# Kernel optimization log

Measured on AMD Instinct MI355X. Metric: run time of the kernel, lower is better.

The kernel has to match this reference:

```python
import jax, jax.numpy as jnp
import numpy as np

N, D, B, NMAX, H = 6144, 512, 16, 512, 8
HD = D // H
LARGE = 1e10
EPS = 1e-5


def setup_inputs() -> dict:
    key = jax.random.key(0)
    ks = jax.random.split(key, 20)
    s = 0.02
    inp = {
        'h': jax.random.normal(ks[0], (N, D), jnp.float32),
        'batch': jnp.sort(jax.random.randint(ks[1], (N,), 0, B)),
        # attention projections (stored as [in, out])
        'Wq': jax.random.normal(ks[2], (D, D), jnp.float32) * s,
        'bq': jnp.zeros((D,), jnp.float32),
        'Wk': jax.random.normal(ks[3], (D, D), jnp.float32) * s,
        'bk': jnp.zeros((D,), jnp.float32),
        'Wv': jax.random.normal(ks[4], (D, D), jnp.float32) * s,
        'bv': jnp.zeros((D,), jnp.float32),
        'Wo': jax.random.normal(ks[5], (D, D), jnp.float32) * s,
        'bo': jnp.zeros((D,), jnp.float32),
        # batchnorm 1 (after attention residual)
        'g1': jnp.ones((D,), jnp.float32),
        'be1': jnp.zeros((D,), jnp.float32),
        # FFN
        'W1': jax.random.normal(ks[6], (D, 2 * D), jnp.float32) * s,
        'b1': jnp.zeros((2 * D,), jnp.float32),
        'W2': jax.random.normal(ks[7], (2 * D, D), jnp.float32) * s,
        'b2': jnp.zeros((D,), jnp.float32),
        # batchnorm 2 (after FFN residual)
        'g2': jnp.ones((D,), jnp.float32),
        'be2': jnp.zeros((D,), jnp.float32),
    }
    return inp


def _batchnorm(x, g, b):
    # BatchNorm1d in training mode: batch statistics over the node dim
    m = jnp.mean(x, axis=0)
    v = jnp.var(x, axis=0)
    return (x - m) * jax.lax.rsqrt(v + EPS) * g + b


def reference(h, batch, Wq, bq, Wk, bk, Wv, bv, Wo, bo, g1, be1, W1, b1, W2, b2, g2, be2):
    # to_dense_batch: batch is sorted graph ids -> position within each graph
    starts = jnp.searchsorted(batch, jnp.arange(B))
    pos = jnp.arange(h.shape[0]) - starts[batch]
    hd = jnp.zeros((B, NMAX, D), h.dtype).at[batch, pos].set(h)
    mask = jnp.zeros((B, NMAX), bool).at[batch, pos].set(True)

    # attention (note reshape splits hidden as [head_dim, head], faithful to torch code)
    q = (hd @ Wq + bq).reshape(B, NMAX, HD, H)
    k = (hd @ Wk + bk).reshape(B, NMAX, HD, H)
    v = (hd @ Wv + bv).reshape(B, NMAX, HD, H)
    score = jnp.einsum('bnfh,bmfh->bnmh', k, q) / (HD ** 0.5)
    score = score - (~mask)[:, None, :, None].astype(score.dtype) * LARGE
    attn = jax.nn.softmax(score, axis=2)
    av = jnp.einsum('bnmh,bmfh->bnfh', attn, v).reshape(B, NMAX, D)
    out = av @ Wo + bo

    # back to flat node list (dense[mask]) + residual + BN
    h_attn = out[batch, pos]
    h_attn = h + h_attn
    h_attn = _batchnorm(h_attn, g1, be1)

    # FFN + residual + BN
    ff = jax.nn.relu(h_attn @ W1 + b1) @ W2 + b2
    return _batchnorm(h_attn + ff, g2, be2)
```

## Files before the change

kernel.cpp:

```cpp
#include <hip/hip_runtime.h>
#include <stdint.h>

#define N_NODES 6144
#define DIM 512
#define NGRAPH 16
#define NHEAD 8
#define EPSV 1e-5f

typedef unsigned short u16;
typedef short s16x4 __attribute__((ext_vector_type(4)));
typedef short s16x8 __attribute__((ext_vector_type(8)));
typedef __bf16 bf16x8 __attribute__((ext_vector_type(8)));
typedef float f32x4 __attribute__((ext_vector_type(4)));

__device__ __forceinline__ u16 f2bf(float f) {
  union { float f; unsigned u; } c{f};
  unsigned u = c.u;
  return (u16)((u + 0x7fffu + ((u >> 16) & 1u)) >> 16);
}
__device__ __forceinline__ float bf2f(u16 v) {
  union { unsigned u; float f; } c{(unsigned)v << 16};
  return c.f;
}

__device__ __forceinline__ f32x4 mfma16(s16x8 a, s16x8 b, f32x4 c) {
  return __builtin_amdgcn_mfma_f32_16x16x32_bf16(
      __builtin_bit_cast(bf16x8, a), __builtin_bit_cast(bf16x8, b), c, 0, 0, 0);
}

__device__ __forceinline__ void gload_lds16(const void* g, void* l) {
  __builtin_amdgcn_global_load_lds(
      (const __attribute__((address_space(1))) unsigned int*)g,
      (__attribute__((address_space(3))) unsigned int*)l, 16, 0, 0);
}

__device__ __forceinline__ s16x8 v_frag_tr(const u16* base, int u16idx) {
  s16x4 lo, hi;
  const __attribute__((address_space(3))) u16* p =
      (const __attribute__((address_space(3))) u16*)(base + u16idx);
  asm volatile("ds_read_b64_tr_b16 %0, %2\n\t"
               "ds_read_b64_tr_b16 %1, %2 offset:128\n\t"
               "s_waitcnt lgkmcnt(0)"
               : "=&v"(lo), "=&v"(hi)
               : "v"(p)
               : "memory");
  __builtin_amdgcn_sched_barrier(0);
  s16x8 r;
  r[0] = lo[0]; r[1] = lo[1]; r[2] = lo[2]; r[3] = lo[3];
  r[4] = hi[0]; r[5] = hi[1]; r[6] = hi[2]; r[7] = hi[3];
  return r;
}

__global__ void prep_kernel(const float* __restrict__ h, const int* __restrict__ batch,
                            const float* __restrict__ Wq, const float* __restrict__ Wk,
                            const float* __restrict__ Wv, const float* __restrict__ Wo,
                            const float* __restrict__ W1, const float* __restrict__ W2,
                            u16* __restrict__ bt_qkv, u16* __restrict__ bt_o,
                            u16* __restrict__ bt_1, u16* __restrict__ bt_2,
                            u16* __restrict__ A0, int* __restrict__ starts) {
  __shared__ float tile[32][33];
  const int bid = blockIdx.x, tid = threadIdx.x;
  if (bid == 0) {
    int g = tid;
    if (g > NGRAPH) return;
    if (g == NGRAPH) { starts[g] = N_NODES; return; }
    int lo = 0, hi = N_NODES;
    while (lo < hi) { int mid = (lo + hi) >> 1; if (batch[mid] < g) lo = mid + 1; else hi = mid; }
    starts[g] = lo;
    return;
  }
  if (bid >= 2049) {
    int i = (bid - 2049) * 256 + tid;
    float4 v = ((const float4*)h)[i];
    ushort4 o = make_ushort4(f2bf(v.x), f2bf(v.y), f2bf(v.z), f2bf(v.w));
    ((ushort4*)A0)[i] = o;
    return;
  }
  const int tx = tid & 31, ty = tid >> 5;
  if (bid <= 768) {
    const int w = (bid - 1) >> 8;
    const float* src = (w == 0) ? Wq : (w == 1) ? Wk : Wv;
    u16* dst = bt_qkv + (size_t)w * 512 * 512;
    const int t = (bid - 1) & 255;
    const int c0 = (t & 15) * 32, r0 = (t >> 4) * 32;
#pragma unroll
    for (int i = 0; i < 32; i += 8) tile[ty + i][tx] = src[(size_t)(r0 + ty + i) * 512 + c0 + tx];
    __syncthreads();
#pragma unroll
    for (int i = 0; i < 32; i += 8) {
      int c = c0 + ty + i;
      int v = ((c & 7) << 6) | (c >> 3);
      dst[(size_t)v * 512 + r0 + tx] = f2bf(tile[tx][ty + i]);
    }
  } else if (bid <= 1024) {
    const int t = bid - 769;
    const int c0 = (t & 15) * 32, j0 = (t >> 4) * 32;
#pragma unroll
    for (int i = 0; i < 32; i += 8) {
      int c = c0 + ty + i;
      int md = ((c & 63) << 3) | (c >> 6);
      tile[ty + i][tx] = Wo[(size_t)md * 512 + j0 + tx];
    }
    __syncthreads();
#pragma unroll
    for (int i = 0; i < 32; i += 8)
      bt_o[(size_t)(j0 + ty + i) * 512 + c0 + tx] = f2bf(tile[tx][ty + i]);
  } else if (bid <= 1536) {
    const int t = bid - 1025;
    const int c0 = (t & 31) * 32, r0 = (t >> 5) * 32;
#pragma unroll
    for (int i = 0; i < 32; i += 8) tile[ty + i][tx] = W1[(size_t)(r0 + ty + i) * 1024 + c0 + tx];
    __syncthreads();
#pragma unroll
    for (int i = 0; i < 32; i += 8) bt_1[(size_t)(c0 + ty + i) * 512 + r0 + tx] = f2bf(tile[tx][ty + i]);
  } else {
    const int t = bid - 1537;
    const int c0 = (t & 15) * 32, r0 = (t >> 4) * 32;
#pragma unroll
    for (int i = 0; i < 32; i += 8) tile[ty + i][tx] = W2[(size_t)(r0 + ty + i) * 512 + c0 + tx];
    __syncthreads();
#pragma unroll
    for (int i = 0; i < 32; i += 8) bt_2[(size_t)(c0 + ty + i) * 1024 + r0 + tx] = f2bf(tile[tx][ty + i]);
  }
}

template <int BM, int BN, int EPI>
__global__ __launch_bounds__(256, 2) void gemm_kernel(
    const u16* __restrict__ A, const u16* __restrict__ Bt,
    const float* __restrict__ bias0, const float* __restrict__ bias1,
    const float* __restrict__ bias2, const float* __restrict__ resf,
    const u16* __restrict__ resb, float2* __restrict__ part,
    u16* __restrict__ oq, u16* __restrict__ ok, u16* __restrict__ ov,
    float* __restrict__ of, u16* __restrict__ ob, int M, int N, int K) {
  constexpr int NW_M = (BM >= 128) ? 2 : 1;
  constexpr int NW_N = 4 / NW_M;
  constexpr int WM = BM / NW_M, WN = BN / NW_N;
  constexpr int FM = WM / 16, FN = WN / 16;
  __shared__ __align__(16) u16 As[BM * 64];
  __shared__ __align__(16) u16 Bs[BN * 64];
  const int tid = threadIdx.x;
  const int lane = tid & 63, wv = tid >> 6;
  const int wm = wv / NW_N, wn = wv % NW_N;
  const int row0 = blockIdx.y * BM, col0 = blockIdx.x * BN;

  f32x4 acc[FM][FN] = {};
  int a_off[FM], b_off[FN];
#pragma unroll
  for (int fm = 0; fm < FM; ++fm) {
    int r = wm * WM + fm * 16 + (lane & 15);
    a_off[fm] = r * 32 + (((lane >> 4) ^ ((r >> 1) & 3)) << 3);
  }
#pragma unroll
  for (int fn = 0; fn < FN; ++fn) {
    int r = wn * WN + fn * 16 + (lane & 15);
    b_off[fn] = r * 32 + (((lane >> 4) ^ ((r >> 1) & 3)) << 3);
  }

  for (int k0 = 0; k0 < K; k0 += 64) {
    __syncthreads();
#pragma unroll
    for (int is = 0; is < BM / 32; ++is) {
      int s = is * 256 + tid;
      int kh = s / (BM * 4);
      int sh = s - kh * (BM * 4);
      int r = sh >> 2;
      int cl = (sh & 3) ^ ((r >> 1) & 3);
      gload_lds16(A + (size_t)(row0 + r) * K + k0 + kh * 32 + cl * 8,
                  (void*)(As + (size_t)(is * 256 + (tid & ~63)) * 8));
    }
#pragma unroll
    for (int is = 0; is < BN / 32; ++is) {
      int s = is * 256 + tid;
      int kh = s / (BN * 4);
      int sh = s - kh * (BN * 4);
      int r = sh >> 2;
      int cl = (sh & 3) ^ ((r >> 1) & 3);
      gload_lds16(Bt + (size_t)(col0 + r) * K + k0 + kh * 32 + cl * 8,
                  (void*)(Bs + (size_t)(is * 256 + (tid & ~63)) * 8));
    }
    __syncthreads();
#pragma unroll
    for (int kh = 0; kh < 2; ++kh) {
      s16x8 af[FM], bfv[FN];
#pragma unroll
      for (int fm = 0; fm < FM; ++fm) af[fm] = *(const s16x8*)(As + kh * (BM * 32) + a_off[fm]);
#pragma unroll
      for (int fn = 0; fn < FN; ++fn) bfv[fn] = *(const s16x8*)(Bs + kh * (BN * 32) + b_off[fn]);
#pragma unroll
      for (int fm = 0; fm < FM; ++fm)
#pragma unroll
        for (int fn = 0; fn < FN; ++fn)
          acc[fm][fn] = mfma16(af[fm], bfv[fn], acc[fm][fn]);
    }
  }

  if constexpr (EPI == 0) {
    const int which = col0 >> 9;
    u16* dst = (which == 0) ? oq : (which == 1) ? ok : ov;
    const float* bias = (which == 0) ? bias0 : (which == 1) ? bias1 : bias2;
#pragma unroll
    for (int fn = 0; fn < FN; ++fn) {
      const int j = col0 + wn * WN + fn * 16 + (lane & 15);
      const int v = j & 511;
      const float bj = bias[((v & 63) << 3) | (v >> 6)];
#pragma unroll
      for (int fm = 0; fm < FM; ++fm) {
        const int ibase = row0 + wm * WM + fm * 16 + ((lane >> 4) << 2);
#pragma unroll
        for (int ii = 0; ii < 4; ++ii)
          dst[(size_t)(ibase + ii) * 512 + v] = f2bf(acc[fm][fn][ii] + bj);
      }
    }
  } else {
#pragma unroll
    for (int fn = 0; fn < FN; ++fn) {
      const int j = col0 + wn * WN + fn * 16 + (lane & 15);
      const float bj = bias0[j];
      float s = 0.f, q = 0.f;
#pragma unroll
      for (int fm = 0; fm < FM; ++fm) {
        const int ibase = row0 + wm * WM + fm * 16 + ((lane >> 4) << 2);
        if constexpr (EPI == 1) {
#pragma unroll
          for (int ii = 0; ii < 4; ++ii) {
            int i = ibase + ii;
            float val = acc[fm][fn][ii] + bj + resf[(size_t)i * N + j];
            ob[(size_t)i * N + j] = f2bf(val);
            s += val; q += val * val;
          }
        } else if constexpr (EPI == 2) {
#pragma unroll
          for (int ii = 0; ii < 4; ++ii) {
            int i = ibase + ii;
            float v = acc[fm][fn][ii] + bj;
            ob[(size_t)i * N + j] = f2bf(v > 0.f ? v : 0.f);
          }
        } else {
#pragma unroll
          for (int ii = 0; ii < 4; ++ii) {
            int i = ibase + ii;
            float val = acc[fm][fn][ii] + bj + bf2f(resb[(size_t)i * N + j]);
            of[(size_t)i * N + j] = val;
            s += val; q += val * val;
          }
        }
      }
      if constexpr (EPI == 1 || EPI == 3) {
        s += __shfl_xor(s, 16); s += __shfl_xor(s, 32);
        q += __shfl_xor(q, 16); q += __shfl_xor(q, 32);
        if ((lane >> 4) == 0) part[(size_t)blockIdx.y * 512 + j] = make_float2(s, q);
      }
    }
  }
}

__global__ __launch_bounds__(256, 2) void attn_kernel(
    const u16* __restrict__ qp, const u16* __restrict__ kp,
    const u16* __restrict__ vp, const int* __restrict__ starts,
    u16* __restrict__ av) {
  __shared__ __align__(16) u16 Qs[32 * 64];
  __shared__ __align__(16) u16 Vs[32 * 64];
  __shared__ __align__(16) u16 Ps[4][512];
  const int idx = blockIdx.x;
  const int rb = idx & 7, hh = (idx >> 3) & 7, b = idx >> 6;
  const int base = starts[b], nb = starts[b + 1] - base;
  const int r0 = rb * 64;
  if (r0 >= nb) return;
  const int tid = threadIdx.x, lane = tid & 63, wv = tid >> 6;
  const int g = lane >> 4;
  const int rloc = r0 + wv * 16 + (lane & 15);
  const u16* krow = kp + (size_t)(base + rloc) * 512 + hh * 64 + (g << 3);
  s16x8 ak0 = *(const s16x8*)(krow);
  s16x8 ak1 = *(const s16x8*)(krow + 32);
  f32x4 acc_av[4] = {};
  float rs[4] = {0.f, 0.f, 0.f, 0.f};
  u16* Pw = Ps[wv];
  const int vm = ((tid & 63) >> 3) * 4 + ((tid >> 1) & 3);
  const int vf = wv * 16 + (tid & 1) * 8;

  for (int m0 = 0; m0 < nb; m0 += 32) {
    __syncthreads();
    {
      int r = tid >> 3, cl = (tid & 7) ^ (r & 7);
      gload_lds16(qp + (size_t)(base + m0 + r) * 512 + hh * 64 + cl * 8,
                  (void*)(Qs + (size_t)(tid & ~63) * 8));
    }
    {
      gload_lds16(vp + (size_t)(base + m0 + vm) * 512 + hh * 64 + vf,
                  (void*)(Vs + (size_t)(tid & ~63) * 8));
    }
    __syncthreads();
#pragma unroll
    for (int ch = 0; ch < 2; ++ch) {
      f32x4 s = {};
#pragma unroll
      for (int kc = 0; kc < 2; ++kc) {
        const int mr = ch * 16 + (lane & 15);
        const int chunk = kc * 4 + g;
        s16x8 bq = *(const s16x8*)(Qs + mr * 64 + ((chunk ^ (mr & 7)) << 3));
        s = mfma16(kc == 0 ? ak0 : ak1, bq, s);
      }
      const int mg = m0 + ch * 16 + (lane & 15);
      const bool valid = mg < nb;
      const int c = ch * 16 + (lane & 15);
#pragma unroll
      for (int ii = 0; ii < 4; ++ii) {
        float pv = valid ? __expf(s[ii] * 0.125f) : 0.f;
        rs[ii] += pv;
        const int r = (g << 2) + ii;
        Pw[r * 32 + (((c >> 3) ^ ((r >> 1) & 3)) << 3) + (c & 7)] = f2bf(pv);
      }
    }
    const int pr = lane & 15;
    s16x8 pa = *(const s16x8*)(Pw + pr * 32 + ((g ^ ((pr >> 1) & 3)) << 3));
#pragma unroll
    for (int fb = 0; fb < 4; ++fb) {
      s16x8 bv = v_frag_tr(Vs, fb * 512 + g * 128 + (lane & 15));
      acc_av[fb] = mfma16(pa, bv, acc_av[fb]);
    }
  }
#pragma unroll
  for (int ii = 0; ii < 4; ++ii) {
    float v = rs[ii];
    v += __shfl_xor(v, 1); v += __shfl_xor(v, 2);
    v += __shfl_xor(v, 4); v += __shfl_xor(v, 8);
    rs[ii] = 1.f / v;
  }
#pragma unroll
  for (int ii = 0; ii < 4; ++ii) {
    const int rl = r0 + wv * 16 + (g << 2) + ii;
    if (rl < nb) {
      const size_t node = base + rl;
#pragma unroll
      for (int fb = 0; fb < 4; ++fb) {
        const int f = fb * 16 + (lane & 15);
        av[node * 512 + hh * 64 + f] = f2bf(acc_av[fb][ii] * rs[ii]);
      }
    }
  }
}

__global__ void bn_fin_kernel(const float2* __restrict__ part, const float* __restrict__ g,
                              const float* __restrict__ be, float2* __restrict__ stats) {
  __shared__ float red_s[8][32];
  __shared__ float red_q[8][32];
  const int t = threadIdx.x;
  const int lc = t & 31, rg = t >> 5;
  const int c = blockIdx.x * 32 + lc;
  float s = 0.f, q = 0.f;
#pragma unroll
  for (int k = 0; k < 12; ++k) {
    float2 v = part[(size_t)(rg + 8 * k) * 512 + c];
    s += v.x; q += v.y;
  }
  red_s[rg][lc] = s; red_q[rg][lc] = q;
  __syncthreads();
  if (rg == 0) {
#pragma unroll
    for (int r = 1; r < 8; ++r) { s += red_s[r][lc]; q += red_q[r][lc]; }
    const float inv = 1.f / (float)N_NODES;
    float m = s * inv, var = q * inv - m * m;
    float sc = g[c] * rsqrtf(var + EPSV);
    stats[c] = make_float2(sc, be[c] - m * sc);
  }
}

__global__ void bn_apply_bf_kernel(const u16* __restrict__ x, const float2* __restrict__ stats,
                                   u16* __restrict__ o) {
  const int i = (blockIdx.x * 256 + threadIdx.x) * 8;
  s16x8 v = *(const s16x8*)(x + i);
  const int c0 = i & 511;
  s16x8 r;
#pragma unroll
  for (int t = 0; t < 8; ++t) {
    float2 st = stats[c0 + t];
    r[t] = (short)f2bf(bf2f((u16)v[t]) * st.x + st.y);
  }
  *(s16x8*)(o + i) = r;
}

__global__ void bn_apply_f32_kernel(float* __restrict__ x, const float2* __restrict__ stats) {
  const int i = (blockIdx.x * 256 + threadIdx.x) * 4;
  float4 v = *(float4*)(x + i);
  const int c = i & 511;
  float2 sa = stats[c], sb = stats[c + 1], sc2 = stats[c + 2], sd = stats[c + 3];
  *(float4*)(x + i) = make_float4(v.x * sa.x + sa.y, v.y * sb.x + sb.y,
                                  v.z * sc2.x + sc2.y, v.w * sd.x + sd.y);
}

extern "C" void kernel_launch(void* const* d_in, const int* in_sizes, int n_in,
                              void* d_out, int out_size, void* d_ws, size_t ws_size,
                              hipStream_t stream) {
  const float* h   = (const float*)d_in[0];
  const int* batch = (const int*)d_in[1];
  const float* Wq = (const float*)d_in[2];  const float* bq = (const float*)d_in[3];
  const float* Wk = (const float*)d_in[4];  const float* bk = (const float*)d_in[5];
  const float* Wv = (const float*)d_in[6];  const float* bv = (const float*)d_in[7];
  const float* Wo = (const float*)d_in[8];  const float* bo = (const float*)d_in[9];
  const float* g1 = (const float*)d_in[10]; const float* be1 = (const float*)d_in[11];
  const float* W1 = (const float*)d_in[12]; const float* b1v = (const float*)d_in[13];
  const float* W2 = (const float*)d_in[14]; const float* b2v = (const float*)d_in[15];
  const float* g2 = (const float*)d_in[16]; const float* be2 = (const float*)d_in[17];
  float* out = (float*)d_out;
  (void)in_sizes; (void)n_in; (void)out_size; (void)ws_size;

  char* ws = (char*)d_ws;
  size_t off = 0;
  auto alloc = [&](size_t bytes) -> void* {
    void* p = ws + off;
    off += (bytes + 255) & ~(size_t)255;
    return p;
  };
  int*    starts = (int*)alloc(17 * 4);
  float2* part1  = (float2*)alloc((size_t)96 * 512 * sizeof(float2));
  float2* part2  = (float2*)alloc((size_t)96 * 512 * sizeof(float2));
  float2* stats1 = (float2*)alloc(512 * sizeof(float2));
  float2* stats2 = (float2*)alloc(512 * sizeof(float2));
  u16* bt_qkv = (u16*)alloc((size_t)1536 * 512 * 2);
  u16* bt_o   = (u16*)alloc((size_t)512 * 512 * 2);
  u16* bt_1   = (u16*)alloc((size_t)1024 * 512 * 2);
  u16* bt_2   = (u16*)alloc((size_t)512 * 1024 * 2);
  u16* A0  = (u16*)alloc((size_t)N_NODES * 512 * 2);
  u16* qp  = (u16*)alloc((size_t)(N_NODES + 64) * 512 * 2);
  u16* kp  = (u16*)alloc((size_t)(N_NODES + 64) * 512 * 2);
  u16* vpb = (u16*)alloc((size_t)(N_NODES + 64) * 512 * 2);
  u16* x1b = (u16*)alloc((size_t)N_NODES * 512 * 2);
  u16* x1n = (u16*)alloc((size_t)N_NODES * 512 * 2);
  u16* av = A0;
  u16* x2 = qp;

  prep_kernel<<<5121, 256, 0, stream>>>(h, batch, Wq, Wk, Wv, Wo, W1, W2,
                                        bt_qkv, bt_o, bt_1, bt_2, A0, starts);
  gemm_kernel<128, 128, 0><<<dim3(12, 48), 256, 0, stream>>>(
      A0, bt_qkv, bq, bk, bv, nullptr, nullptr, nullptr, qp, kp, vpb,
      nullptr, nullptr, N_NODES, 1536, 512);
  attn_kernel<<<NGRAPH * NHEAD * 8, 256, 0, stream>>>(qp, kp, vpb, starts, av);
  gemm_kernel<64, 128, 1><<<dim3(4, 96), 256, 0, stream>>>(
      av, bt_o, bo, nullptr, nullptr, h, nullptr, part1, nullptr, nullptr, nullptr,
      nullptr, x1b, N_NODES, 512, 512);
  bn_fin_kernel<<<16, 256, 0, stream>>>(part1, g1, be1, stats1);
  bn_apply_bf_kernel<<<1536, 256, 0, stream>>>(x1b, stats1, x1n);
  gemm_kernel<128, 128, 2><<<dim3(8, 48), 256, 0, stream>>>(
      x1n, bt_1, b1v, nullptr, nullptr, nullptr, nullptr, nullptr, nullptr, nullptr,
      nullptr, nullptr, x2, N_NODES, 1024, 512);
  gemm_kernel<64, 128, 3><<<dim3(4, 96), 256, 0, stream>>>(
      x2, bt_2, b2v, nullptr, nullptr, nullptr, x1n, part2, nullptr, nullptr, nullptr,
      out, nullptr, N_NODES, 512, 1024);
  bn_fin_kernel<<<16, 256, 0, stream>>>(part2, g2, be2, stats2);
  bn_apply_f32_kernel<<<3072, 256, 0, stream>>>(out, stats2);
}
```

Baseline: 114.4 us.

## Double-buffer GEMM shared memory tiles to overlap global loads with MFMA

Doubles the LDS tiles for A and B and restructures the k-loop. Each step loads all fragments of the current tile into registers, issues the async global-to-LDS load for the next tile into the other buffer, then runs the MFMAs, so memory latency overlaps with compute and one barrier per iteration is dropped. This doubles LDS use and raises register pressure, which may lower occupancy under launch_bounds(256,2).

```diff
diff --git a/kernel.cpp b/kernel.cpp
--- a/kernel.cpp
+++ b/kernel.cpp
@@ -136,8 +136,9 @@
   constexpr int NW_N = 4 / NW_M;
   constexpr int WM = BM / NW_M, WN = BN / NW_N;
   constexpr int FM = WM / 16, FN = WN / 16;
-  __shared__ __align__(16) u16 As[BM * 64];
-  __shared__ __align__(16) u16 Bs[BN * 64];
+  constexpr int ASZ = BM * 64, BSZ = BN * 64;
+  __shared__ __align__(16) u16 As[2 * ASZ];
+  __shared__ __align__(16) u16 Bs[2 * BSZ];
   const int tid = threadIdx.x;
   const int lane = tid & 63, wv = tid >> 6;
   const int wm = wv / NW_N, wn = wv % NW_N;
@@ -156,8 +157,7 @@
     b_off[fn] = r * 32 + (((lane >> 4) ^ ((r >> 1) & 3)) << 3);
   }
 
-  for (int k0 = 0; k0 < K; k0 += 64) {
-    __syncthreads();
+  auto stage = [&](int buf, int k0) {
 #pragma unroll
     for (int is = 0; is < BM / 32; ++is) {
       int s = is * 256 + tid;
@@ -166,7 +166,7 @@
       int r = sh >> 2;
       int cl = (sh & 3) ^ ((r >> 1) & 3);
       gload_lds16(A + (size_t)(row0 + r) * K + k0 + kh * 32 + cl * 8,
-                  (void*)(As + (size_t)(is * 256 + (tid & ~63)) * 8));
+                  (void*)(As + buf * ASZ + (size_t)(is * 256 + (tid & ~63)) * 8));
     }
 #pragma unroll
     for (int is = 0; is < BN / 32; ++is) {
@@ -176,22 +176,35 @@
       int r = sh >> 2;
       int cl = (sh & 3) ^ ((r >> 1) & 3);
       gload_lds16(Bt + (size_t)(col0 + r) * K + k0 + kh * 32 + cl * 8,
-                  (void*)(Bs + (size_t)(is * 256 + (tid & ~63)) * 8));
-    }
-    __syncthreads();
+                  (void*)(Bs + buf * BSZ + (size_t)(is * 256 + (tid & ~63)) * 8));
+    }
+  };
+
+  stage(0, 0);
+  __syncthreads();
+  const int nt = K >> 6;
+  int cur = 0;
+  for (int t = 0; t < nt; ++t) {
+    s16x8 af[2][FM], bfv[2][FN];
 #pragma unroll
     for (int kh = 0; kh < 2; ++kh) {
-      s16x8 af[FM], bfv[FN];
-#pragma unroll
-      for (int fm = 0; fm < FM; ++fm) af[fm] = *(const s16x8*)(As + kh * (BM * 32) + a_off[fm]);
-#pragma unroll
-      for (int fn = 0; fn < FN; ++fn) bfv[fn] = *(const s16x8*)(Bs + kh * (BN * 32) + b_off[fn]);
 #pragma unroll
       for (int fm = 0; fm < FM; ++fm)
+        af[kh][fm] = *(const s16x8*)(As + cur * ASZ + kh * (BM * 32) + a_off[fm]);
+#pragma unroll
+      for (int fn = 0; fn < FN; ++fn)
+        bfv[kh][fn] = *(const s16x8*)(Bs + cur * BSZ + kh * (BN * 32) + b_off[fn]);
+    }
+    if (t + 1 < nt) stage(cur ^ 1, (t + 1) << 6);
+#pragma unroll
+    for (int kh = 0; kh < 2; ++kh)
+#pragma unroll
+      for (int fm = 0; fm < FM; ++fm)
 #pragma unroll
         for (int fn = 0; fn < FN; ++fn)
-          acc[fm][fn] = mfma16(af[fm], bfv[fn], acc[fm][fn]);
-    }
+          acc[fm][fn] = mfma16(af[kh][fm], bfv[kh][fn], acc[fm][fn]);
+    __syncthreads();
+    cur ^= 1;
   }
 
   if constexpr (EPI == 0) {
```

Measured after the change: 114.9 us. About the same (+0.4%).

## Fold BN1 affine into FFN W1 weights and bias, apply in W2 residual

Applied to the files above, without the earlier changes.

Removes the separate BN1 apply pass. The BN1 scale is folded into the transposed W1 weights and its shift into a new fused bias for the first FFN GEMM, so that GEMM reads the un-normalized x1b directly. The second FFN GEMM applies the BN1 affine to the residual in its epilogue. The QKV GEMM also moves to 128x192 tiles with a per-fragment output selector, which changes the grid from 12x48 to 8x48. Rounding differs slightly, since the scaled weights are re-rounded to bf16 and the normalization is no longer applied to bf16 activations.

```diff
diff --git a/kernel.cpp b/kernel.cpp
--- a/kernel.cpp
+++ b/kernel.cpp
@@ -129,7 +129,8 @@
     const u16* __restrict__ A, const u16* __restrict__ Bt,
     const float* __restrict__ bias0, const float* __restrict__ bias1,
     const float* __restrict__ bias2, const float* __restrict__ resf,
-    const u16* __restrict__ resb, float2* __restrict__ part,
+    const u16* __restrict__ resb, const float2* __restrict__ stats,
+    float2* __restrict__ part,
     u16* __restrict__ oq, u16* __restrict__ ok, u16* __restrict__ ov,
     float* __restrict__ of, u16* __restrict__ ob, int M, int N, int K) {
   constexpr int NW_M = (BM >= 128) ? 2 : 1;
@@ -195,12 +196,12 @@
   }
 
   if constexpr (EPI == 0) {
-    const int which = col0 >> 9;
-    u16* dst = (which == 0) ? oq : (which == 1) ? ok : ov;
-    const float* bias = (which == 0) ? bias0 : (which == 1) ? bias1 : bias2;
 #pragma unroll
     for (int fn = 0; fn < FN; ++fn) {
       const int j = col0 + wn * WN + fn * 16 + (lane & 15);
+      const int which = j >> 9;
+      u16* dst = (which == 0) ? oq : (which == 1) ? ok : ov;
+      const float* bias = (which == 0) ? bias0 : (which == 1) ? bias1 : bias2;
       const int v = j & 511;
       const float bj = bias[((v & 63) << 3) | (v >> 6)];
 #pragma unroll
@@ -236,10 +237,11 @@
             ob[(size_t)i * N + j] = f2bf(v > 0.f ? v : 0.f);
           }
         } else {
+          const float2 st = stats[j];
 #pragma unroll
           for (int ii = 0; ii < 4; ++ii) {
             int i = ibase + ii;
-            float val = acc[fm][fn][ii] + bj + bf2f(resb[(size_t)i * N + j]);
+            float val = acc[fm][fn][ii] + bj + (bf2f(resb[(size_t)i * N + j]) * st.x + st.y);
             of[(size_t)i * N + j] = val;
             s += val; q += val * val;
           }
@@ -365,18 +367,26 @@
   }
 }
 
-__global__ void bn_apply_bf_kernel(const u16* __restrict__ x, const float2* __restrict__ stats,
-                                   u16* __restrict__ o) {
-  const int i = (blockIdx.x * 256 + threadIdx.x) * 8;
-  s16x8 v = *(const s16x8*)(x + i);
-  const int c0 = i & 511;
-  s16x8 r;
+__global__ void bn1_fold_kernel(u16* __restrict__ bt_1, const float* __restrict__ b1,
+                                const float2* __restrict__ stats1, float* __restrict__ b1f) {
+  const int tid = threadIdx.x, lane = tid & 63, wv = tid >> 6;
+  const int j = blockIdx.x * 4 + wv;
+  u16* row = bt_1 + (size_t)j * 512 + lane * 8;
+  s16x8 v = *(const s16x8*)row;
+  s16x8 o;
+  float dot = 0.f;
 #pragma unroll
   for (int t = 0; t < 8; ++t) {
-    float2 st = stats[c0 + t];
-    r[t] = (short)f2bf(bf2f((u16)v[t]) * st.x + st.y);
-  }
-  *(s16x8*)(o + i) = r;
+    float2 st = stats1[lane * 8 + t];
+    float w = bf2f((u16)v[t]);
+    o[t] = (short)f2bf(w * st.x);
+    dot += w * st.y;
+  }
+  *(s16x8*)row = o;
+  dot += __shfl_xor(dot, 1);  dot += __shfl_xor(dot, 2);
+  dot += __shfl_xor(dot, 4);  dot += __shfl_xor(dot, 8);
+  dot += __shfl_xor(dot, 16); dot += __shfl_xor(dot, 32);
+  if (lane == 0) b1f[j] = b1[j] + dot;
 }
 
 __global__ void bn_apply_f32_kernel(float* __restrict__ x, const float2* __restrict__ stats) {
@@ -416,6 +426,7 @@
   float2* part2  = (float2*)alloc((size_t)96 * 512 * sizeof(float2));
   float2* stats1 = (float2*)alloc(512 * sizeof(float2));
   float2* stats2 = (float2*)alloc(512 * sizeof(float2));
+  float*  b1f    = (float*)alloc(1024 * sizeof(float));
   u16* bt_qkv = (u16*)alloc((size_t)1536 * 512 * 2);
   u16* bt_o   = (u16*)alloc((size_t)512 * 512 * 2);
   u16* bt_1   = (u16*)alloc((size_t)1024 * 512 * 2);
@@ -425,27 +436,26 @@
   u16* kp  = (u16*)alloc((size_t)(N_NODES + 64) * 512 * 2);
   u16* vpb = (u16*)alloc((size_t)(N_NODES + 64) * 512 * 2);
   u16* x1b = (u16*)alloc((size_t)N_NODES * 512 * 2);
-  u16* x1n = (u16*)alloc((size_t)N_NODES * 512 * 2);
   u16* av = A0;
   u16* x2 = qp;
 
   prep_kernel<<<5121, 256, 0, stream>>>(h, batch, Wq, Wk, Wv, Wo, W1, W2,
                                         bt_qkv, bt_o, bt_1, bt_2, A0, starts);
-  gemm_kernel<128, 128, 0><<<dim3(12, 48), 256, 0, stream>>>(
-      A0, bt_qkv, bq, bk, bv, nullptr, nullptr, nullptr, qp, kp, vpb,
+  gemm_kernel<128, 192, 0><<<dim3(8, 48), 256, 0, stream>>>(
+      A0, bt_qkv, bq, bk, bv, nullptr, nullptr, nullptr, nullptr, qp, kp, vpb,
       nullptr, nullptr, N_NODES, 1536, 512);
   attn_kernel<<<NGRAPH * NHEAD * 8, 256, 0, stream>>>(qp, kp, vpb, starts, av);
   gemm_kernel<64, 128, 1><<<dim3(4, 96), 256, 0, stream>>>(
-      av, bt_o, bo, nullptr, nullptr, h, nullptr, part1, nullptr, nullptr, nullptr,
-      nullptr, x1b, N_NODES, 512, 512);
+      av, bt_o, bo, nullptr, nullptr, h, nullptr, nullptr, part1,
+      nullptr, nullptr, nullptr, nullptr, x1b, N_NODES, 512, 512);
   bn_fin_kernel<<<16, 256, 0, stream>>>(part1, g1, be1, stats1);
-  bn_apply_bf_kernel<<<1536, 256, 0, stream>>>(x1b, stats1, x1n);
+  bn1_fold_kernel<<<256, 256, 0, stream>>>(bt_1, b1v, stats1, b1f);
   gemm_kernel<128, 128, 2><<<dim3(8, 48), 256, 0, stream>>>(
-      x1n, bt_1, b1v, nullptr, nullptr, nullptr, nullptr, nullptr, nullptr, nullptr,
-      nullptr, nullptr, x2, N_NODES, 1024, 512);
+      x1b, bt_1, b1f, nullptr, nullptr, nullptr, nullptr, nullptr, nullptr,
+      nullptr, nullptr, nullptr, nullptr, x2, N_NODES, 1024, 512);
   gemm_kernel<64, 128, 3><<<dim3(4, 96), 256, 0, stream>>>(
-      x2, bt_2, b2v, nullptr, nullptr, nullptr, x1n, part2, nullptr, nullptr, nullptr,
-      out, nullptr, N_NODES, 512, 1024);
+      x2, bt_2, b2v, nullptr, nullptr, nullptr, x1b, stats1, part2,
+      nullptr, nullptr, nullptr, out, nullptr, N_NODES, 512, 1024);
   bn_fin_kernel<<<16, 256, 0, stream>>>(part2, g2, be2, stats2);
   bn_apply_f32_kernel<<<3072, 256, 0, stream>>>(out, stats2);
 }
```

Result: no change. 113.8 us (-0.5%).
